# Kernel tuning notes

Hardware: AMD Instinct MI355X
Metric: run time of the kernel (lower is better)

The kernel has to match this reference:

```python
import jax, jax.numpy as jnp
import numpy as np

H, OC = 64, 32  # hidden_channels, out_channels
N0, N1, N2, N3 = 65536, 16384, 4096, 1024
K3, K2 = 27, 8  # kernel taps: 3^3 stride-1 conv, 2^3 stride-2 conv


def _spconv(feat, nmap, W, b):
    # gather-GEMM sparse conv: feat [N_in,C], nmap [N_out,K] indices, W [K,C,D]
    g = feat[nmap]                       # [N_out, K, C]
    return jnp.einsum('nkc,kcd->nd', g, W) + b


def setup_inputs() -> dict:
    key = jax.random.key(0)
    ks = jax.random.split(key, 16)
    f32 = jnp.float32
    d = {
        'x': jax.random.normal(ks[0], (N0, H), f32),
        'Wg0': jax.random.normal(ks[1], (OC, H), f32) / np.sqrt(OC),
        'bg0': jnp.zeros((H,), f32),
        'Wg1': jax.random.normal(ks[2], (OC, H), f32) / np.sqrt(OC),
        'bg1': jnp.zeros((H,), f32),
        'Wout': jax.random.normal(ks[3], (H, OC), f32) / np.sqrt(H),
        'bout': jnp.zeros((OC,), f32),
        'WA': jax.random.normal(ks[4], (K3, H, H), f32) / np.sqrt(K3 * H),
        'bA': jnp.zeros((H,), f32),
        'WB': jax.random.normal(ks[5], (K3, H, H), f32) / np.sqrt(K3 * H),
        'bB': jnp.zeros((H,), f32),
        'WD': jax.random.normal(ks[6], (K2, H, H), f32) / np.sqrt(K2 * H),
        'bD': jnp.zeros((H,), f32),
        'WC': jax.random.normal(ks[7], (K3, H, H), f32) / np.sqrt(K3 * H),
        'bC': jnp.zeros((H,), f32),
        'nmap0': jax.random.randint(ks[8], (N0, K3), 0, N0, jnp.int32),
        'nmap1': jax.random.randint(ks[9], (N1, K3), 0, N1, jnp.int32),
        'nmap2': jax.random.randint(ks[10], (N2, K3), 0, N2, jnp.int32),
        'nmap3': jax.random.randint(ks[11], (N3, K3), 0, N3, jnp.int32),
        'nd0': jax.random.randint(ks[12], (N1, K2), 0, N0, jnp.int32),
        'nd1': jax.random.randint(ks[13], (N2, K2), 0, N1, jnp.int32),
        'nd2': jax.random.randint(ks[14], (N3, K2), 0, N2, jnp.int32),
    }
    return d


def reference(x, Wg0, bg0, Wg1, bg1, Wout, bout, WA, bA, WB, bB, WD, bD, WC, bC,
              nmap0, nmap1, nmap2, nmap3, nd0, nd1, nd2):
    nmaps = [nmap0, nmap1, nmap2, nmap3]
    nds = [nd0, nd1, nd2]
    outs = []
    cx = x
    hx = cx @ Wout + bout            # block_out (hidden -> out_channels)
    outs.append(hx)
    for s in range(3):               # unrolled recurrent while-loop (3 scales)
        # sub-step 0: gate + two stride-1 sparse convs at same coords
        g = jax.nn.sigmoid(hx @ Wg0 + bg0)
        cx = g * cx
        cx = jax.nn.relu(_spconv(cx, nmaps[s], WA, bA))
        cx = jax.nn.relu(_spconv(cx, nmaps[s], WB, bB))
        hx = cx @ Wout + bout
        outs.append(hx)
        # sub-step 1: gate + stride-2 downsample conv + stride-1 conv
        g = jax.nn.sigmoid(hx @ Wg1 + bg1)
        cx = g * cx
        cx = jax.nn.relu(_spconv(cx, nds[s], WD, bD))      # N_s -> N_{s+1}
        cx = jax.nn.relu(_spconv(cx, nmaps[s + 1], WC, bC))
        hx = cx @ Wout + bout
        outs.append(hx)
    return tuple(outs)
```

## Files before the change

### kernel.cpp

```cpp
#include <hip/hip_runtime.h>
#include <hip/hip_bf16.h>

typedef __attribute__((ext_vector_type(8))) short short8;
typedef __attribute__((ext_vector_type(4))) float f32x4;

#define N0 65536
#define N1 16384
#define N2 4096
#define N3 1024

__global__ void prep_w4(const float* __restrict__ A, const float* __restrict__ B,
                        const float* __restrict__ C, const float* __restrict__ D,
                        __hip_bfloat16* __restrict__ dst, int total)
{
    int i = blockIdx.x * 256 + threadIdx.x;
    if (i >= total) return;
    int k = i >> 12, r = i & 4095, d = r >> 6, c = r & 63;
    const float* src; int kl;
    if (k < 27)      { src = A; kl = k; }
    else if (k < 54) { src = B; kl = k - 27; }
    else if (k < 81) { src = C; kl = k - 54; }
    else             { src = D; kl = k - 81; }
    dst[i] = __float2bfloat16(src[(kl << 12) + (c << 6) + d]);
}

__global__ __launch_bounds__(256) void spconv_mfma(
    const __hip_bfloat16* __restrict__ feat, const int* __restrict__ nmap,
    const __hip_bfloat16* __restrict__ Wt, void* __restrict__ outp,
    const float* __restrict__ bias, int Nout, int K, int mode)
{
    __shared__ short Abuf[2][64 * 64];
    __shared__ short Bbuf[2][64 * 64];
    __shared__ int jl[27 * 64];

    const int t = threadIdx.x;
    const int w = t >> 6, l = t & 63;
    const int lr = l & 15, lh = l >> 4;
    const int row0 = blockIdx.x * 64;
    const int per = (K + gridDim.y - 1) / gridDim.y;
    const int kb0 = blockIdx.y * per;
    const int nk = min(K, kb0 + per) - kb0;

    for (int i = t; i < nk * 64; i += 256) {
        int k = i >> 6, r = i & 63;
        jl[i] = nmap[(size_t)(row0 + r) * K + (kb0 + k)];
    }
    __syncthreads();

    const int rr0 = (w << 4) + (l >> 3);
    const int qq = (l & 7) ^ (l >> 3);

    auto stage = [&](int buf, int k) {
        const __hip_bfloat16* Wk = Wt + (size_t)(kb0 + k) * 4096;
#pragma unroll
        for (int i = 0; i < 2; ++i) {
            int rr = rr0 + (i << 3);
            int j = jl[(k << 6) + rr];
            __builtin_amdgcn_global_load_lds(
                (const __attribute__((address_space(1))) void*)(feat + ((size_t)j << 6) + (qq << 3)),
                (__attribute__((address_space(3))) void*)&Abuf[buf][(w << 10) + (i << 9)],
                16, 0, 0);
            __builtin_amdgcn_global_load_lds(
                (const __attribute__((address_space(1))) void*)(Wk + (rr << 6) + (qq << 3)),
                (__attribute__((address_space(3))) void*)&Bbuf[buf][(w << 10) + (i << 9)],
                16, 0, 0);
        }
    };

    f32x4 acc[4] = {};
    const int arow = (w << 4) + lr;

#define COMPUTE(cur_)                                                            \
    {                                                                            \
        const short* Ab = Abuf[cur_];                                            \
        const short* Bb = Bbuf[cur_];                                            \
        _Pragma("unroll")                                                        \
        for (int kk = 0; kk < 2; ++kk) {                                         \
            int q = (kk << 2) + lh;                                              \
            short8 a = *(const short8*)&Ab[(arow << 6) + ((q ^ (arow & 7)) << 3)];\
            _Pragma("unroll")                                                    \
            for (int ct = 0; ct < 4; ++ct) {                                     \
                int dr = (ct << 4) + lr;                                         \
                short8 b = *(const short8*)&Bb[(dr << 6) + ((q ^ (dr & 7)) << 3)];\
                acc[ct] = __builtin_amdgcn_mfma_f32_16x16x32_bf16(a, b, acc[ct], 0, 0, 0); \
            }                                                                    \
        }                                                                        \
    }

    stage(0, 0);

    int cur = 0;
    for (int k = 0; k < nk; ++k) {
        if (k + 1 < nk) {
            stage(cur ^ 1, k + 1);
            asm volatile("s_waitcnt vmcnt(4)" ::: "memory");
        } else {
            asm volatile("s_waitcnt vmcnt(0)" ::: "memory");
        }
        asm volatile("s_barrier" ::: "memory");
        COMPUTE(cur);
        asm volatile("s_barrier" ::: "memory");
        cur ^= 1;
    }
#undef COMPUTE

    if (mode == 1) {
        float* o32 = (float*)outp + (size_t)blockIdx.y * ((size_t)Nout << 6);
#pragma unroll
        for (int ct = 0; ct < 4; ++ct) {
            int col = (ct << 4) + lr;
#pragma unroll
            for (int rr = 0; rr < 4; ++rr) {
                int row = row0 + (w << 4) + (lh << 2) + rr;
                o32[((size_t)row << 6) + col] = acc[ct][rr];
            }
        }
    } else {
        __hip_bfloat16* ob = (__hip_bfloat16*)outp;
#pragma unroll
        for (int ct = 0; ct < 4; ++ct) {
            int col = (ct << 4) + lr;
            float bv = (mode == 2) ? bias[col] : 0.f;
#pragma unroll
            for (int rr = 0; rr < 4; ++rr) {
                int row = row0 + (w << 4) + (lh << 2) + rr;
                float v = acc[ct][rr];
                if (mode == 2) v = fmaxf(v + bv, 0.f);
                ob[((size_t)row << 6) + col] = __float2bfloat16(v);
            }
        }
    }
}

__global__ void reduce_relu_bf(const float* __restrict__ in, const float* __restrict__ bias,
                               __hip_bfloat16* __restrict__ outb, int nv, int ch)
{
    int i = blockIdx.x * blockDim.x + threadIdx.x;
    if (i >= nv) return;
    const float4* in4 = (const float4*)in;
    float4 s = in4[i];
    for (int c = 1; c < ch; ++c) {
        float4 v = in4[(size_t)c * nv + i];
        s.x += v.x; s.y += v.y; s.z += v.z; s.w += v.w;
    }
    int cb = (i << 2) & 63;
    ushort4 o;
    o.x = __builtin_bit_cast(unsigned short, __float2bfloat16(fmaxf(s.x + bias[cb + 0], 0.f)));
    o.y = __builtin_bit_cast(unsigned short, __float2bfloat16(fmaxf(s.y + bias[cb + 1], 0.f)));
    o.z = __builtin_bit_cast(unsigned short, __float2bfloat16(fmaxf(s.z + bias[cb + 2], 0.f)));
    o.w = __builtin_bit_cast(unsigned short, __float2bfloat16(fmaxf(s.w + bias[cb + 3], 0.f)));
    ((ushort4*)outb)[i] = o;
}

__global__ __launch_bounds__(256) void epi_full(
    const void* __restrict__ srcp, int smode, int ch, const float* __restrict__ bconv,
    const float* __restrict__ Wout, const float* __restrict__ bout,
    const float* __restrict__ Wg, const float* __restrict__ bg,
    float* __restrict__ hx_out, __hip_bfloat16* __restrict__ gout, int N)
{
    __shared__ float Woutl[64 * 32];
    __shared__ float Wgl[32 * 64];
    __shared__ float boutl[32];
    __shared__ float bgl[64];
    __shared__ float bcl[64];

    const int t = threadIdx.x;
    for (int i = t; i < 2048; i += 256) {
        int r = i >> 5, col = i & 31;
        int q = col >> 2, e = col & 3;
        Woutl[(r << 5) + ((q ^ (r >> 3)) << 2) + e] = Wout[i];
        Wgl[i] = Wg[i];
    }
    if (t < 32) boutl[t] = bout[t];
    if (t >= 64 && t < 128) bgl[t - 64] = bg[t - 64];
    if (t >= 128 && t < 192) bcl[t - 128] = bconv ? bconv[t - 128] : 0.f;
    __syncthreads();

    const int g = t & 7;
    const int row = blockIdx.x * 32 + (t >> 3);
    const int c0 = g << 3;

    float tv[8];
    if (smode == 0) {
        const ushort4* sb = (const ushort4*)((const __hip_bfloat16*)srcp + ((size_t)row << 6) + c0);
        ushort4 v0 = sb[0], v1 = sb[1];
        tv[0] = __bfloat162float(__builtin_bit_cast(__hip_bfloat16, v0.x));
        tv[1] = __bfloat162float(__builtin_bit_cast(__hip_bfloat16, v0.y));
        tv[2] = __bfloat162float(__builtin_bit_cast(__hip_bfloat16, v0.z));
        tv[3] = __bfloat162float(__builtin_bit_cast(__hip_bfloat16, v0.w));
        tv[4] = __bfloat162float(__builtin_bit_cast(__hip_bfloat16, v1.x));
        tv[5] = __bfloat162float(__builtin_bit_cast(__hip_bfloat16, v1.y));
        tv[6] = __bfloat162float(__builtin_bit_cast(__hip_bfloat16, v1.z));
        tv[7] = __bfloat162float(__builtin_bit_cast(__hip_bfloat16, v1.w));
    } else {
        const float4* sf = (const float4*)((const float*)srcp + ((size_t)row << 6) + c0);
        float4 a = sf[0], b = sf[1];
        if (smode == 3) {
            const size_t cs = (size_t)N * 16;
            for (int c = 1; c < ch; ++c) {
                float4 u = sf[c * cs], v = sf[c * cs + 1];
                a.x += u.x; a.y += u.y; a.z += u.z; a.w += u.w;
                b.x += v.x; b.y += v.y; b.z += v.z; b.w += v.w;
            }
        }
        tv[0] = a.x; tv[1] = a.y; tv[2] = a.z; tv[3] = a.w;
        tv[4] = b.x; tv[5] = b.y; tv[6] = b.z; tv[7] = b.w;
    }
    if (smode != 2) {
#pragma unroll
        for (int i = 0; i < 8; ++i) tv[i] = fmaxf(tv[i] + bcl[c0 + i], 0.f);
    }

    float ph[32];
#pragma unroll
    for (int d = 0; d < 32; ++d) ph[d] = 0.f;
#pragma unroll
    for (int i = 0; i < 8; ++i) {
        float tc = tv[i];
        const float* wr = &Woutl[(c0 + i) << 5];
#pragma unroll
        for (int q = 0; q < 8; ++q) {
            f32x4 wv = *(const f32x4*)&wr[(q ^ g) << 2];
            ph[q * 4 + 0] = fmaf(tc, wv[0], ph[q * 4 + 0]);
            ph[q * 4 + 1] = fmaf(tc, wv[1], ph[q * 4 + 1]);
            ph[q * 4 + 2] = fmaf(tc, wv[2], ph[q * 4 + 2]);
            ph[q * 4 + 3] = fmaf(tc, wv[3], ph[q * 4 + 3]);
        }
    }
#pragma unroll
    for (int m = 1; m < 8; m <<= 1) {
#pragma unroll
        for (int d = 0; d < 32; ++d) ph[d] += __shfl_xor(ph[d], m);
    }
#pragma unroll
    for (int d = 0; d < 32; ++d) ph[d] += boutl[d];

    {
        float* ho = hx_out + ((size_t)row << 5);
#pragma unroll
        for (int G = 0; G < 8; ++G)
            if (g == G) {
                float4 v = {ph[G * 4 + 0], ph[G * 4 + 1], ph[G * 4 + 2], ph[G * 4 + 3]};
                ((float4*)ho)[G] = v;
            }
    }

    float ga[8];
#pragma unroll
    for (int j = 0; j < 8; ++j) ga[j] = bgl[c0 + j];
#pragma unroll
    for (int d = 0; d < 32; ++d) {
        float hd = ph[d];
        const float* wr = &Wgl[(d << 6) + c0];
        f32x4 w0 = *(const f32x4*)&wr[0];
        f32x4 w1 = *(const f32x4*)&wr[4];
        ga[0] = fmaf(hd, w0[0], ga[0]); ga[1] = fmaf(hd, w0[1], ga[1]);
        ga[2] = fmaf(hd, w0[2], ga[2]); ga[3] = fmaf(hd, w0[3], ga[3]);
        ga[4] = fmaf(hd, w1[0], ga[4]); ga[5] = fmaf(hd, w1[1], ga[5]);
        ga[6] = fmaf(hd, w1[2], ga[6]); ga[7] = fmaf(hd, w1[3], ga[7]);
    }
    {
        unsigned short ob[8];
#pragma unroll
        for (int j = 0; j < 8; ++j) {
            float gg = 1.f / (1.f + __expf(-ga[j]));
            ob[j] = __builtin_bit_cast(unsigned short, __float2bfloat16(gg * tv[j]));
        }
        ushort4* go = (ushort4*)(gout + ((size_t)row << 6) + c0);
        ushort4 o0 = {ob[0], ob[1], ob[2], ob[3]};
        ushort4 o1 = {ob[4], ob[5], ob[6], ob[7]};
        go[0] = o0; go[1] = o1;
    }
}

extern "C" void kernel_launch(void* const* d_in, const int* in_sizes, int n_in,
                              void* d_out, int out_size, void* d_ws, size_t ws_size,
                              hipStream_t stream)
{
    const float* x    = (const float*)d_in[0];
    const float* Wg0  = (const float*)d_in[1];
    const float* bg0  = (const float*)d_in[2];
    const float* Wg1  = (const float*)d_in[3];
    const float* bg1  = (const float*)d_in[4];
    const float* Wout = (const float*)d_in[5];
    const float* bout = (const float*)d_in[6];
    const float* WA   = (const float*)d_in[7];
    const float* bA   = (const float*)d_in[8];
    const float* WB   = (const float*)d_in[9];
    const float* bB   = (const float*)d_in[10];
    const float* WD   = (const float*)d_in[11];
    const float* bD   = (const float*)d_in[12];
    const float* WC   = (const float*)d_in[13];
    const float* bC   = (const float*)d_in[14];
    const int* nmap[4] = {(const int*)d_in[15], (const int*)d_in[16],
                          (const int*)d_in[17], (const int*)d_in[18]};
    const int* ndm[3]  = {(const int*)d_in[19], (const int*)d_in[20],
                          (const int*)d_in[21]};

    float* out = (float*)d_out;
    __hip_bfloat16* featbf0 = (__hip_bfloat16*)d_ws;
    __hip_bfloat16* featbf1 = featbf0 + (size_t)N0 * 64;
    __hip_bfloat16* convbf  = featbf1 + (size_t)N0 * 64;
    float* conv32 = (float*)(convbf + (size_t)N0 * 64);
    __hip_bfloat16* WAt = (__hip_bfloat16*)(conv32 + (size_t)N2 * 64 * 8);
    __hip_bfloat16* WBt = WAt + 27 * 4096;
    __hip_bfloat16* WCt = WBt + 27 * 4096;
    __hip_bfloat16* WDt = WCt + 27 * 4096;

    const int Ns[4] = {N0, N1, N2, N3};
    size_t off[7];
    off[0] = 0;
    off[1] = off[0] + (size_t)N0 * 32;
    off[2] = off[1] + (size_t)N0 * 32;
    off[3] = off[2] + (size_t)N1 * 32;
    off[4] = off[3] + (size_t)N1 * 32;
    off[5] = off[4] + (size_t)N2 * 32;
    off[6] = off[5] + (size_t)N2 * 32;

    hipLaunchKernelGGL(prep_w4, dim3((89 * 4096 + 255) / 256), dim3(256), 0, stream,
                       WA, WB, WC, WD, WAt, 89 * 4096);

    auto chunks = [&](int Nout, int K) -> int {
        if (Nout >= 16384) return 1;
        if (Nout == 4096) return (K == 27) ? 4 : 2;
        return (K == 27) ? 7 : 4;
    };
    auto conv = [&](const __hip_bfloat16* fin, const int* nm,
                    const __hip_bfloat16* Wt, int Nout, int K,
                    const float* bias2, void* dst, int mode) -> int {
        int ch = chunks(Nout, K);
        if (ch > 1) {
            hipLaunchKernelGGL(spconv_mfma, dim3(Nout / 64, ch), dim3(256), 0, stream,
                               fin, nm, Wt, (void*)conv32, (const float*)nullptr,
                               Nout, K, 1);
            return ch;
        }
        hipLaunchKernelGGL(spconv_mfma, dim3(Nout / 64, 1), dim3(256), 0, stream,
                           fin, nm, Wt, dst, bias2, Nout, K, mode);
        return 0;
    };

    hipLaunchKernelGGL(epi_full, dim3(N0 / 32), dim3(256), 0, stream,
                       (const void*)x, 2, 1, (const float*)nullptr, Wout, bout, Wg0, bg0,
                       out + off[0], featbf0, N0);

    for (int s = 0; s < 3; ++s) {
        int N = Ns[s], Nn = Ns[s + 1];

        int mA = conv(featbf0, nmap[s], WAt, N, 27, bA, featbf1, 2);
        if (mA)
            hipLaunchKernelGGL(reduce_relu_bf, dim3((N * 16 + 255) / 256), dim3(256), 0, stream,
                               conv32, bA, featbf1, N * 16, mA);
        int mB = conv(featbf1, nmap[s], WBt, N, 27, nullptr, convbf, 0);
        hipLaunchKernelGGL(epi_full, dim3(N / 32), dim3(256), 0, stream,
                           mB ? (const void*)conv32 : (const void*)convbf, mB ? 3 : 0, mB, bB,
                           Wout, bout, Wg1, bg1, out + off[s * 2 + 1], featbf0, N);

        int mD = conv(featbf0, ndm[s], WDt, Nn, 8, bD, featbf1, 2);
        if (mD)
            hipLaunchKernelGGL(reduce_relu_bf, dim3((Nn * 16 + 255) / 256), dim3(256), 0, stream,
                               conv32, bD, featbf1, Nn * 16, mD);
        int mC = conv(featbf1, nmap[s + 1], WCt, Nn, 27, nullptr, convbf, 0);
        hipLaunchKernelGGL(epi_full, dim3(Nn / 32), dim3(256), 0, stream,
                           mC ? (const void*)conv32 : (const void*)convbf, mC ? 3 : 0, mC, bC,
                           Wout, bout, Wg0, bg0, out + off[s * 2 + 2], featbf0, Nn);
    }
}
```

Measured before the change: 274.8 us.

## Fuse output projection and gating epilogue into sparse conv kernel, drop split-K

The epilogue (bias+ReLU, the Wout projection to hx, the sigmoid gate and the gated feature write) now runs inside the spconv kernel as mode 3. Its weights are prefetched into LDS during the last K step. The split-K path with fp32 partial buffers and reduce kernels is removed, so every conv runs as one pass over all K taps. This cuts launches and intermediate global traffic. In exchange the small scales (N=4096, 1024) get few blocks (64 and 16), which may leave most of the GPU idle.

```diff
diff --git a/kernel.cpp b/kernel.cpp
--- a/kernel.cpp
+++ b/kernel.cpp
@@ -9,41 +9,73 @@
 #define N2 4096
 #define N3 1024
 
-__global__ void prep_w4(const float* __restrict__ A, const float* __restrict__ B,
-                        const float* __restrict__ C, const float* __restrict__ D,
-                        __hip_bfloat16* __restrict__ dst, int total)
+__device__ __forceinline__ float bfu(unsigned short u) {
+    unsigned int x = ((unsigned int)u) << 16;
+    return __builtin_bit_cast(float, x);
+}
+__device__ __forceinline__ unsigned short fbf(float f) {
+    return __builtin_bit_cast(unsigned short, __float2bfloat16(f));
+}
+
+__global__ void prep_all(const float* __restrict__ A, const float* __restrict__ B,
+                         const float* __restrict__ C, const float* __restrict__ D,
+                         const float* __restrict__ Wg0, const float* __restrict__ Wg1,
+                         const float* __restrict__ bB, const float* __restrict__ bC,
+                         const float* __restrict__ bout, const float* __restrict__ bg0,
+                         const float* __restrict__ bg1,
+                         __hip_bfloat16* __restrict__ Wt,
+                         __hip_bfloat16* __restrict__ Wgb,
+                         float* __restrict__ pack)
 {
     int i = blockIdx.x * 256 + threadIdx.x;
-    if (i >= total) return;
-    int k = i >> 12, r = i & 4095, d = r >> 6, c = r & 63;
-    const float* src; int kl;
-    if (k < 27)      { src = A; kl = k; }
-    else if (k < 54) { src = B; kl = k - 27; }
-    else if (k < 81) { src = C; kl = k - 54; }
-    else             { src = D; kl = k - 81; }
-    dst[i] = __float2bfloat16(src[(kl << 12) + (c << 6) + d]);
+    if (i < 89 * 4096) {
+        int k = i >> 12, r = i & 4095, d = r >> 6, c = r & 63;
+        const float* src; int kl;
+        if (k < 27)      { src = A; kl = k; }
+        else if (k < 54) { src = B; kl = k - 27; }
+        else if (k < 81) { src = C; kl = k - 54; }
+        else             { src = D; kl = k - 81; }
+        Wt[i] = __float2bfloat16(src[(kl << 12) + (c << 6) + d]);
+        return;
+    }
+    int j = i - 89 * 4096;
+    if (j < 2048) { Wgb[j] = __float2bfloat16(Wg1[j]); return; }
+    j -= 2048;
+    if (j < 2048) { Wgb[2048 + j] = __float2bfloat16(Wg0[j]); return; }
+    j -= 2048;
+    if (j < 160) {
+        pack[j] = (j < 64) ? bB[j] : (j < 96) ? bout[j - 64] : bg1[j - 96];
+        return;
+    }
+    j -= 160;
+    if (j < 160) {
+        pack[160 + j] = (j < 64) ? bC[j] : (j < 96) ? bout[j - 64] : bg0[j - 96];
+    }
 }
 
 __global__ __launch_bounds__(256) void spconv_mfma(
     const __hip_bfloat16* __restrict__ feat, const int* __restrict__ nmap,
-    const __hip_bfloat16* __restrict__ Wt, void* __restrict__ outp,
-    const float* __restrict__ bias, int Nout, int K, int mode)
+    const __hip_bfloat16* __restrict__ Wt, __hip_bfloat16* __restrict__ outp,
+    const float* __restrict__ bias, int Nout, int K, int mode,
+    const float* __restrict__ Woutg, const __hip_bfloat16* __restrict__ Wgb,
+    const float* __restrict__ pack, float* __restrict__ hx_out,
+    __hip_bfloat16* __restrict__ gout)
 {
-    __shared__ short Abuf[2][64 * 64];
-    __shared__ short Bbuf[2][64 * 64];
-    __shared__ int jl[27 * 64];
+    __shared__ int ldsm[10240];
+    short* AbufS = (short*)ldsm;
+    short* BbufS = (short*)(ldsm + 4096);
+    int*   jl    = ldsm + 8192;
+    short* WgL   = (short*)(ldsm + 8192);
+    float* packL = (float*)(ldsm + 8192 + 1024);
 
     const int t = threadIdx.x;
     const int w = t >> 6, l = t & 63;
     const int lr = l & 15, lh = l >> 4;
     const int row0 = blockIdx.x * 64;
-    const int per = (K + gridDim.y - 1) / gridDim.y;
-    const int kb0 = blockIdx.y * per;
-    const int nk = min(K, kb0 + per) - kb0;
-
-    for (int i = t; i < nk * 64; i += 256) {
+
+    for (int i = t; i < K * 64; i += 256) {
         int k = i >> 6, r = i & 63;
-        jl[i] = nmap[(size_t)(row0 + r) * K + (kb0 + k)];
+        jl[i] = nmap[(size_t)(row0 + r) * K + k];
     }
     __syncthreads();
 
@@ -51,20 +83,43 @@
     const int qq = (l & 7) ^ (l >> 3);
 
     auto stage = [&](int buf, int k) {
-        const __hip_bfloat16* Wk = Wt + (size_t)(kb0 + k) * 4096;
+        const __hip_bfloat16* Wk = Wt + (size_t)k * 4096;
 #pragma unroll
         for (int i = 0; i < 2; ++i) {
             int rr = rr0 + (i << 3);
             int j = jl[(k << 6) + rr];
             __builtin_amdgcn_global_load_lds(
                 (const __attribute__((address_space(1))) void*)(feat + ((size_t)j << 6) + (qq << 3)),
-                (__attribute__((address_space(3))) void*)&Abuf[buf][(w << 10) + (i << 9)],
+                (__attribute__((address_space(3))) void*)(AbufS + buf * 4096 + (w << 10) + (i << 9)),
                 16, 0, 0);
             __builtin_amdgcn_global_load_lds(
                 (const __attribute__((address_space(1))) void*)(Wk + (rr << 6) + (qq << 3)),
-                (__attribute__((address_space(3))) void*)&Bbuf[buf][(w << 10) + (i << 9)],
+                (__attribute__((address_space(3))) void*)(BbufS + buf * 4096 + (w << 10) + (i << 9)),
                 16, 0, 0);
         }
+    };
+
+    auto stage_epi = [&](int buf) {
+        short* dstW = BbufS + buf * 4096;
+#pragma unroll
+        for (int i = 0; i < 2; ++i) {
+            int s = t + i * 256;
+            int r = s >> 3, qp = s & 7;
+            int q = qp ^ (r >> 4);
+            __builtin_amdgcn_global_load_lds(
+                (const __attribute__((address_space(1))) void*)(Woutg + (r << 5) + (q << 2)),
+                (__attribute__((address_space(3))) void*)(dstW + (w << 9) + (i << 11)),
+                16, 0, 0);
+        }
+        __builtin_amdgcn_global_load_lds(
+            (const __attribute__((address_space(1))) void*)(Wgb + (t << 3)),
+            (__attribute__((address_space(3))) void*)(WgL + (w << 9)),
+            16, 0, 0);
+        if (t < 40)
+            __builtin_amdgcn_global_load_lds(
+                (const __attribute__((address_space(1))) void*)(pack + (t << 2)),
+                (__attribute__((address_space(3))) void*)packL,
+                16, 0, 0);
     };
 
     f32x4 acc[4] = {};
@@ -72,8 +127,8 @@
 
 #define COMPUTE(cur_)                                                            \
     {                                                                            \
-        const short* Ab = Abuf[cur_];                                            \
-        const short* Bb = Bbuf[cur_];                                            \
+        const short* Ab = AbufS + (cur_) * 4096;                                 \
+        const short* Bb = BbufS + (cur_) * 4096;                                 \
         _Pragma("unroll")                                                        \
         for (int kk = 0; kk < 2; ++kk) {                                         \
             int q = (kk << 2) + lh;                                              \
@@ -90,11 +145,12 @@
     stage(0, 0);
 
     int cur = 0;
-    for (int k = 0; k < nk; ++k) {
-        if (k + 1 < nk) {
+    for (int k = 0; k < K; ++k) {
+        if (k + 1 < K) {
             stage(cur ^ 1, k + 1);
             asm volatile("s_waitcnt vmcnt(4)" ::: "memory");
         } else {
+            if (mode == 3) stage_epi(cur ^ 1);
             asm volatile("s_waitcnt vmcnt(0)" ::: "memory");
         }
         asm volatile("s_barrier" ::: "memory");
@@ -104,19 +160,7 @@
     }
 #undef COMPUTE
 
-    if (mode == 1) {
-        float* o32 = (float*)outp + (size_t)blockIdx.y * ((size_t)Nout << 6);
-#pragma unroll
-        for (int ct = 0; ct < 4; ++ct) {
-            int col = (ct << 4) + lr;
-#pragma unroll
-            for (int rr = 0; rr < 4; ++rr) {
-                int row = row0 + (w << 4) + (lh << 2) + rr;
-                o32[((size_t)row << 6) + col] = acc[ct][rr];
-            }
-        }
-    } else {
-        __hip_bfloat16* ob = (__hip_bfloat16*)outp;
+    if (mode != 3) {
 #pragma unroll
         for (int ct = 0; ct < 4; ++ct) {
             int col = (ct << 4) + lr;
@@ -126,30 +170,104 @@
                 int row = row0 + (w << 4) + (lh << 2) + rr;
                 float v = acc[ct][rr];
                 if (mode == 2) v = fmaxf(v + bv, 0.f);
-                ob[((size_t)row << 6) + col] = __float2bfloat16(v);
+                outp[((size_t)row << 6) + col] = __float2bfloat16(v);
             }
         }
-    }
-}
-
-__global__ void reduce_relu_bf(const float* __restrict__ in, const float* __restrict__ bias,
-                               __hip_bfloat16* __restrict__ outb, int nv, int ch)
-{
-    int i = blockIdx.x * blockDim.x + threadIdx.x;
-    if (i >= nv) return;
-    const float4* in4 = (const float4*)in;
-    float4 s = in4[i];
-    for (int c = 1; c < ch; ++c) {
-        float4 v = in4[(size_t)c * nv + i];
-        s.x += v.x; s.y += v.y; s.z += v.z; s.w += v.w;
-    }
-    int cb = (i << 2) & 63;
-    ushort4 o;
-    o.x = __builtin_bit_cast(unsigned short, __float2bfloat16(fmaxf(s.x + bias[cb + 0], 0.f)));
-    o.y = __builtin_bit_cast(unsigned short, __float2bfloat16(fmaxf(s.y + bias[cb + 1], 0.f)));
-    o.z = __builtin_bit_cast(unsigned short, __float2bfloat16(fmaxf(s.z + bias[cb + 2], 0.f)));
-    o.w = __builtin_bit_cast(unsigned short, __float2bfloat16(fmaxf(s.w + bias[cb + 3], 0.f)));
-    ((ushort4*)outb)[i] = o;
+        return;
+    }
+
+    short* tl = AbufS;
+    float* WoutL = (float*)(BbufS + cur * 4096);
+
+#pragma unroll
+    for (int ct = 0; ct < 4; ++ct) {
+        int col = (ct << 4) + lr;
+        float bv = packL[col];
+#pragma unroll
+        for (int rr = 0; rr < 4; ++rr) {
+            int rl = (w << 4) + (lh << 2) + rr;
+            float v = fmaxf(acc[ct][rr] + bv, 0.f);
+            tl[rl * 72 + col] = (short)fbf(v);
+        }
+    }
+    __syncthreads();
+
+    const int g4 = t & 3, rloc = t >> 2;
+    const short* trow = tl + rloc * 72 + (g4 << 4);
+    float tv[16];
+    {
+        short8 u0 = *(const short8*)trow;
+        short8 u1 = *(const short8*)(trow + 8);
+#pragma unroll
+        for (int j = 0; j < 8; ++j) {
+            tv[j]     = bfu((unsigned short)u0[j]);
+            tv[8 + j] = bfu((unsigned short)u1[j]);
+        }
+    }
+    float ph[32];
+#pragma unroll
+    for (int d = 0; d < 32; ++d) ph[d] = 0.f;
+#pragma unroll
+    for (int i = 0; i < 16; ++i) {
+        float tc = tv[i];
+        const float* wrow = WoutL + (((g4 << 4) + i) << 5);
+#pragma unroll
+        for (int q = 0; q < 8; ++q) {
+            f32x4 wv = *(const f32x4*)&wrow[(q ^ g4) << 2];
+            ph[q * 4 + 0] = fmaf(tc, wv[0], ph[q * 4 + 0]);
+            ph[q * 4 + 1] = fmaf(tc, wv[1], ph[q * 4 + 1]);
+            ph[q * 4 + 2] = fmaf(tc, wv[2], ph[q * 4 + 2]);
+            ph[q * 4 + 3] = fmaf(tc, wv[3], ph[q * 4 + 3]);
+        }
+    }
+#pragma unroll
+    for (int m = 1; m < 4; m <<= 1) {
+#pragma unroll
+        for (int d = 0; d < 32; ++d) ph[d] += __shfl_xor(ph[d], m);
+    }
+#pragma unroll
+    for (int d = 0; d < 32; ++d) ph[d] += packL[64 + d];
+
+    {
+        float* ho = hx_out + ((size_t)(row0 + rloc) << 5);
+#pragma unroll
+        for (int G = 0; G < 4; ++G)
+            if (g4 == G) {
+                float4 v0 = {ph[G * 8 + 0], ph[G * 8 + 1], ph[G * 8 + 2], ph[G * 8 + 3]};
+                float4 v1 = {ph[G * 8 + 4], ph[G * 8 + 5], ph[G * 8 + 6], ph[G * 8 + 7]};
+                ((float4*)ho)[G * 2 + 0] = v0;
+                ((float4*)ho)[G * 2 + 1] = v1;
+            }
+    }
+
+    float ga[16];
+#pragma unroll
+    for (int j = 0; j < 16; ++j) ga[j] = packL[96 + (g4 << 4) + j];
+#pragma unroll
+    for (int d = 0; d < 32; ++d) {
+        float hd = ph[d];
+        const short* wg = WgL + (d << 6) + (g4 << 4);
+        short8 w0 = *(const short8*)wg;
+        short8 w1 = *(const short8*)(wg + 8);
+#pragma unroll
+        for (int j = 0; j < 8; ++j) {
+            ga[j]     = fmaf(hd, bfu((unsigned short)w0[j]), ga[j]);
+            ga[8 + j] = fmaf(hd, bfu((unsigned short)w1[j]), ga[8 + j]);
+        }
+    }
+    {
+        short8 o0, o1;
+#pragma unroll
+        for (int j = 0; j < 8; ++j) {
+            float g0 = 1.f / (1.f + __expf(-ga[j]));
+            float g1 = 1.f / (1.f + __expf(-ga[8 + j]));
+            o0[j] = (short)fbf(g0 * tv[j]);
+            o1[j] = (short)fbf(g1 * tv[8 + j]);
+        }
+        short* go = (short*)gout + ((size_t)(row0 + rloc) << 6) + (g4 << 4);
+        *(short8*)go = o0;
+        *(short8*)(go + 8) = o1;
+    }
 }
 
 __global__ __launch_bounds__(256) void epi_full(
@@ -184,25 +302,11 @@
     if (smode == 0) {
         const ushort4* sb = (const ushort4*)((const __hip_bfloat16*)srcp + ((size_t)row << 6) + c0);
         ushort4 v0 = sb[0], v1 = sb[1];
-        tv[0] = __bfloat162float(__builtin_bit_cast(__hip_bfloat16, v0.x));
-        tv[1] = __bfloat162float(__builtin_bit_cast(__hip_bfloat16, v0.y));
-        tv[2] = __bfloat162float(__builtin_bit_cast(__hip_bfloat16, v0.z));
-        tv[3] = __bfloat162float(__builtin_bit_cast(__hip_bfloat16, v0.w));
-        tv[4] = __bfloat162float(__builtin_bit_cast(__hip_bfloat16, v1.x));
-        tv[5] = __bfloat162float(__builtin_bit_cast(__hip_bfloat16, v1.y));
-        tv[6] = __bfloat162float(__builtin_bit_cast(__hip_bfloat16, v1.z));
-        tv[7] = __bfloat162float(__builtin_bit_cast(__hip_bfloat16, v1.w));
+        tv[0] = bfu(v0.x); tv[1] = bfu(v0.y); tv[2] = bfu(v0.z); tv[3] = bfu(v0.w);
+        tv[4] = bfu(v1.x); tv[5] = bfu(v1.y); tv[6] = bfu(v1.z); tv[7] = bfu(v1.w);
     } else {
         const float4* sf = (const float4*)((const float*)srcp + ((size_t)row << 6) + c0);
         float4 a = sf[0], b = sf[1];
-        if (smode == 3) {
-            const size_t cs = (size_t)N * 16;
-            for (int c = 1; c < ch; ++c) {
-                float4 u = sf[c * cs], v = sf[c * cs + 1];
-                a.x += u.x; a.y += u.y; a.z += u.z; a.w += u.w;
-                b.x += v.x; b.y += v.y; b.z += v.z; b.w += v.w;
-            }
-        }
         tv[0] = a.x; tv[1] = a.y; tv[2] = a.z; tv[3] = a.w;
         tv[4] = b.x; tv[5] = b.y; tv[6] = b.z; tv[7] = b.w;
     }
@@ -264,7 +368,7 @@
 #pragma unroll
         for (int j = 0; j < 8; ++j) {
             float gg = 1.f / (1.f + __expf(-ga[j]));
-            ob[j] = __builtin_bit_cast(unsigned short, __float2bfloat16(gg * tv[j]));
+            ob[j] = fbf(gg * tv[j]);
         }
         ushort4* go = (ushort4*)(gout + ((size_t)row << 6) + c0);
         ushort4 o0 = {ob[0], ob[1], ob[2], ob[3]};
@@ -300,12 +404,12 @@
     float* out = (float*)d_out;
     __hip_bfloat16* featbf0 = (__hip_bfloat16*)d_ws;
     __hip_bfloat16* featbf1 = featbf0 + (size_t)N0 * 64;
-    __hip_bfloat16* convbf  = featbf1 + (size_t)N0 * 64;
-    float* conv32 = (float*)(convbf + (size_t)N0 * 64);
-    __hip_bfloat16* WAt = (__hip_bfloat16*)(conv32 + (size_t)N2 * 64 * 8);
+    __hip_bfloat16* WAt = featbf1 + (size_t)N0 * 64;
     __hip_bfloat16* WBt = WAt + 27 * 4096;
     __hip_bfloat16* WCt = WBt + 27 * 4096;
     __hip_bfloat16* WDt = WCt + 27 * 4096;
+    __hip_bfloat16* Wgb = WDt + 8 * 4096;
+    float* packw = (float*)(Wgb + 4096);
 
     const int Ns[4] = {N0, N1, N2, N3};
     size_t off[7];
@@ -317,27 +421,27 @@
     off[5] = off[4] + (size_t)N2 * 32;
     off[6] = off[5] + (size_t)N2 * 32;
 
-    hipLaunchKernelGGL(prep_w4, dim3((89 * 4096 + 255) / 256), dim3(256), 0, stream,
-                       WA, WB, WC, WD, WAt, 89 * 4096);
-
-    auto chunks = [&](int Nout, int K) -> int {
-        if (Nout >= 16384) return 1;
-        if (Nout == 4096) return (K == 27) ? 4 : 2;
-        return (K == 27) ? 7 : 4;
+    hipLaunchKernelGGL(prep_all, dim3((89 * 4096 + 4416 + 255) / 256), dim3(256), 0, stream,
+                       WA, WB, WC, WD, Wg0, Wg1, bB, bC, bout, bg0, bg1,
+                       WAt, Wgb, packw);
+
+    auto conv2 = [&](const __hip_bfloat16* fin, const int* nm,
+                     const __hip_bfloat16* Wt, int Nout, int K,
+                     const float* bias2, __hip_bfloat16* dst) {
+        hipLaunchKernelGGL(spconv_mfma, dim3(Nout / 64), dim3(256), 0, stream,
+                           fin, nm, Wt, dst, bias2, Nout, K, 2,
+                           (const float*)nullptr, (const __hip_bfloat16*)nullptr,
+                           (const float*)nullptr, (float*)nullptr,
+                           (__hip_bfloat16*)nullptr);
     };
-    auto conv = [&](const __hip_bfloat16* fin, const int* nm,
-                    const __hip_bfloat16* Wt, int Nout, int K,
-                    const float* bias2, void* dst, int mode) -> int {
-        int ch = chunks(Nout, K);
-        if (ch > 1) {
-            hipLaunchKernelGGL(spconv_mfma, dim3(Nout / 64, ch), dim3(256), 0, stream,
-                               fin, nm, Wt, (void*)conv32, (const float*)nullptr,
-                               Nout, K, 1);
-            return ch;
-        }
-        hipLaunchKernelGGL(spconv_mfma, dim3(Nout / 64, 1), dim3(256), 0, stream,
-                           fin, nm, Wt, dst, bias2, Nout, K, mode);
-        return 0;
+    auto conv3 = [&](const __hip_bfloat16* fin, const int* nm,
+                     const __hip_bfloat16* Wt, int Nout, int K,
+                     const float* packp, const __hip_bfloat16* Wgbp,
+                     float* hx, __hip_bfloat16* gdst) {
+        hipLaunchKernelGGL(spconv_mfma, dim3(Nout / 64), dim3(256), 0, stream,
+                           fin, nm, Wt, (__hip_bfloat16*)nullptr,
+                           (const float*)nullptr, Nout, K, 3,
+                           Wout, Wgbp, packp, hx, gdst);
     };
 
     hipLaunchKernelGGL(epi_full, dim3(N0 / 32), dim3(256), 0, stream,
@@ -347,22 +451,11 @@
     for (int s = 0; s < 3; ++s) {
         int N = Ns[s], Nn = Ns[s + 1];
 
-        int mA = conv(featbf0, nmap[s], WAt, N, 27, bA, featbf1, 2);
-        if (mA)
-            hipLaunchKernelGGL(reduce_relu_bf, dim3((N * 16 + 255) / 256), dim3(256), 0, stream,
-                               conv32, bA, featbf1, N * 16, mA);
-        int mB = conv(featbf1, nmap[s], WBt, N, 27, nullptr, convbf, 0);
-        hipLaunchKernelGGL(epi_full, dim3(N / 32), dim3(256), 0, stream,
-                           mB ? (const void*)conv32 : (const void*)convbf, mB ? 3 : 0, mB, bB,
-                           Wout, bout, Wg1, bg1, out + off[s * 2 + 1], featbf0, N);
-
-        int mD = conv(featbf0, ndm[s], WDt, Nn, 8, bD, featbf1, 2);
-        if (mD)
-            hipLaunchKernelGGL(reduce_relu_bf, dim3((Nn * 16 + 255) / 256), dim3(256), 0, stream,
-                               conv32, bD, featbf1, Nn * 16, mD);
-        int mC = conv(featbf1, nmap[s + 1], WCt, Nn, 27, nullptr, convbf, 0);
-        hipLaunchKernelGGL(epi_full, dim3(Nn / 32), dim3(256), 0, stream,
-                           mC ? (const void*)conv32 : (const void*)convbf, mC ? 3 : 0, mC, bC,
-                           Wout, bout, Wg0, bg0, out + off[s * 2 + 2], featbf0, Nn);
-    }
-}
+        conv2(featbf0, nmap[s], WAt, N, 27, bA, featbf1);
+        conv3(featbf1, nmap[s], WBt, N, 27, packw, Wgb, out + off[s * 2 + 1], featbf0);
+
+        conv2(featbf0, ndm[s], WDt, Nn, 8, bD, featbf1);
+        conv3(featbf1, nmap[s + 1], WCt, Nn, 27, packw + 160, Wgb + 2048,
+              out + off[s * 2 + 2], featbf0);
+    }
+}
```

Measured after the change: 300.2 us. 9.2% more time.
